# Optimization experiments

Hardware: AMD Instinct MI355X
Metric: run time of the kernel (lower is better)

## Reference

```python
import jax, jax.numpy as jnp
import numpy as np

VOCAB, B, T, H, E = 32000, 32, 128, 128, 128

def setup_inputs() -> dict:
    key = jax.random.key(0)
    ks = jax.random.split(key, 10)
    s = 0.05
    return {
        "inputs": jax.random.randint(ks[0], (B, T), 0, VOCAB, dtype=jnp.int32),
        "emb": jax.random.normal(ks[1], (VOCAB, E), jnp.float32) * s,
        "W0": jax.random.normal(ks[2], (E, 4 * H), jnp.float32) * s,
        "U0": jax.random.normal(ks[3], (H, 4 * H), jnp.float32) * s,
        "b0": jnp.zeros((4 * H,), jnp.float32),
        "W1": jax.random.normal(ks[4], (H, 4 * H), jnp.float32) * s,
        "U1": jax.random.normal(ks[5], (H, 4 * H), jnp.float32) * s,
        "b1": jnp.zeros((4 * H,), jnp.float32),
        "Wd": jax.random.normal(ks[6], (H, VOCAB), jnp.float32) * s,
        "bd": jnp.zeros((VOCAB,), jnp.float32),
    }

def _lstm_cell(x, h, c, W, U, b):
    # Keras LSTMCell gate order: i, f, c(candidate), o
    z = x @ W + h @ U + b  # [B, 4H]
    zi, zf, zc, zo = jnp.split(z, 4, axis=-1)
    i = jax.nn.sigmoid(zi)
    f = jax.nn.sigmoid(zf)
    o = jax.nn.sigmoid(zo)
    c_new = f * c + i * jnp.tanh(zc)
    h_new = o * jnp.tanh(c_new)
    return h_new, c_new

def reference(inputs, emb, W0, U0, b0, W1, U1, b1, Wd, bd):
    x = emb[inputs]  # [B, T, E]
    xt = jnp.transpose(x, (1, 0, 2))  # [T, B, E]
    zeros = jnp.zeros((x.shape[0], H), x.dtype)
    init = (zeros, zeros, zeros, zeros)  # h0, c0, h1, c1

    def step(carry, x_t):
        h0, c0, h1, c1 = carry
        h0, c0 = _lstm_cell(x_t, h0, c0, W0, U0, b0)
        h1, c1 = _lstm_cell(h0, h1, c1, W1, U1, b1)
        return (h0, c0, h1, c1), h1

    _, ys = jax.lax.scan(step, init, xt)  # ys: [T, B, H]
    y = jnp.transpose(ys, (1, 0, 2))  # [B, T, H]
    logits = y @ Wd + bd  # [B, T, VOCAB]
    return logits
```

## Files before the change

kernel.cpp:

```cpp
#include <hip/hip_runtime.h>
#include <math.h>

#define BB 32
#define TT 128
#define EE 128
#define HD 128
#define G4 512
#define NV 32000

typedef _Float16 f16x2 __attribute__((ext_vector_type(2)));
typedef _Float16 f16x8 __attribute__((ext_vector_type(8)));
typedef float    f32x4 __attribute__((ext_vector_type(4)));

__global__ __launch_bounds__(256) void k_prep(
    const int* __restrict__ inputs, const float* __restrict__ emb,
    const float* __restrict__ W0, const float* __restrict__ b0,
    float* __restrict__ Z0x,
    const float* __restrict__ Wd, _Float16* __restrict__ Whi, _Float16* __restrict__ Wlo)
{
    if (blockIdx.x < 2000) {
        const int g = blockIdx.x * 256 + threadIdx.x;
        const int chunk = g >> 6;
        const int lane = g & 63;
        const int ntile = chunk >> 2;
        const int kstep = chunk & 3;
        const int n = ntile * 16 + (lane & 15);
        const int kb = kstep * 32 + (lane >> 4) * 8;
        _Float16 hi[8], lo[8];
        #pragma unroll
        for (int j = 0; j < 8; ++j) {
            float v = Wd[(size_t)(kb + j) * NV + n];
            hi[j] = (_Float16)v;
            lo[j] = (_Float16)(v - (float)hi[j]);
        }
        *(float4*)&Whi[(size_t)chunk * 512 + lane * 8] = *(const float4*)hi;
        *(float4*)&Wlo[(size_t)chunk * 512 + lane * 8] = *(const float4*)lo;
        return;
    }
    __shared__ float xs[8][EE];
    const int r0 = (blockIdx.x - 2000) * 8;
    const int tid = threadIdx.x;
    for (int i = tid; i < 8 * EE; i += 256) {
        int r = i >> 7, e = i & 127;
        int tok = inputs[r0 + r];
        xs[r][e] = emb[tok * EE + e];
    }
    __syncthreads();
    const int c2 = tid * 2;
    float2 bb2 = *(const float2*)&b0[c2];
    float acc[8][2];
    #pragma unroll
    for (int r = 0; r < 8; ++r) { acc[r][0] = bb2.x; acc[r][1] = bb2.y; }
    for (int e = 0; e < EE; ++e) {
        float2 w = *(const float2*)&W0[e * G4 + c2];
        #pragma unroll
        for (int r = 0; r < 8; ++r) {
            float x = xs[r][e];
            acc[r][0] = fmaf(x, w.x, acc[r][0]);
            acc[r][1] = fmaf(x, w.y, acc[r][1]);
        }
    }
    #pragma unroll
    for (int r = 0; r < 8; ++r) {
        float2 o2; o2.x = acc[r][0]; o2.y = acc[r][1];
        *(float2*)&Z0x[(size_t)(r0 + r) * G4 + c2] = o2;
    }
}

__global__ __launch_bounds__(512, 2) void k_lstm_f(
    const float* __restrict__ Z0x,
    const float* __restrict__ U0, const float* __restrict__ W1,
    const float* __restrict__ U1, const float* __restrict__ b1,
    float* __restrict__ y)
{
    const int b = blockIdx.x;
    const int tid = threadIdx.x;

    __shared__ _Float16 h0p[HD];
    __shared__ _Float16 h1p[HD];
    __shared__ float zb[G4];
    __shared__ float zu[G4];

    f16x2 u0c[64], w1c[64], u1c[64];
    #pragma unroll
    for (int e2 = 0; e2 < 64; ++e2) {
        u0c[e2] = f16x2{(_Float16)U0[(2 * e2) * G4 + tid], (_Float16)U0[(2 * e2 + 1) * G4 + tid]};
        w1c[e2] = f16x2{(_Float16)W1[(2 * e2) * G4 + tid], (_Float16)W1[(2 * e2 + 1) * G4 + tid]};
        u1c[e2] = f16x2{(_Float16)U1[(2 * e2) * G4 + tid], (_Float16)U1[(2 * e2 + 1) * G4 + tid]};
    }

    const float b1c = b1[tid];
    const float* __restrict__ zrow = Z0x + (size_t)b * TT * G4 + tid;

    float c0 = 0.f, c1 = 0.f;
    if (tid < HD) { h0p[tid] = (_Float16)0.f; h1p[tid] = (_Float16)0.f; }
    __syncthreads();

    const f16x2* h0v = (const f16x2*)h0p;
    const f16x2* h1v = (const f16x2*)h1p;

    for (int t = 0; t < TT; ++t) {
        float a0a = zrow[(size_t)t * G4], a0b = 0.f;
        float aua = 0.f, aub = 0.f;
        #pragma unroll
        for (int e2 = 0; e2 < 64; e2 += 2) {
            a0a = __builtin_amdgcn_fdot2(h0v[e2],     u0c[e2],     a0a, false);
            a0b = __builtin_amdgcn_fdot2(h0v[e2 + 1], u0c[e2 + 1], a0b, false);
            aua = __builtin_amdgcn_fdot2(h1v[e2],     u1c[e2],     aua, false);
            aub = __builtin_amdgcn_fdot2(h1v[e2 + 1], u1c[e2 + 1], aub, false);
        }
        zb[tid] = a0a + a0b;
        zu[tid] = aua + aub;
        __syncthreads();

        if (tid < HD) {
            float zi = zb[tid], zf = zb[HD + tid], zc = zb[2 * HD + tid], zo = zb[3 * HD + tid];
            float ig = 1.f / (1.f + expf(-zi));
            float fg = 1.f / (1.f + expf(-zf));
            float og = 1.f / (1.f + expf(-zo));
            c0 = fg * c0 + ig * tanhf(zc);
            h0p[tid] = (_Float16)(og * tanhf(c0));
        }
        __syncthreads();

        float a1a = b1c + zu[tid], a1b = 0.f;
        #pragma unroll
        for (int e2 = 0; e2 < 64; e2 += 2) {
            a1a = __builtin_amdgcn_fdot2(h0v[e2],     w1c[e2],     a1a, false);
            a1b = __builtin_amdgcn_fdot2(h0v[e2 + 1], w1c[e2 + 1], a1b, false);
        }
        zb[tid] = a1a + a1b;
        __syncthreads();

        if (tid < HD) {
            float zi = zb[tid], zf = zb[HD + tid], zc = zb[2 * HD + tid], zo = zb[3 * HD + tid];
            float ig = 1.f / (1.f + expf(-zi));
            float fg = 1.f / (1.f + expf(-zf));
            float og = 1.f / (1.f + expf(-zo));
            c1 = fg * c1 + ig * tanhf(zc);
            float hn = og * tanhf(c1);
            h1p[tid] = (_Float16)hn;
            y[(size_t)(b * TT + t) * HD + tid] = hn;
        }
        __syncthreads();
    }
}

__global__ __launch_bounds__(256) void k_ysplit(
    const float* __restrict__ y, _Float16* __restrict__ yhi, _Float16* __restrict__ ylo)
{
    const int g = blockIdx.x * 256 + threadIdx.x;
    const int chunk = g >> 6;
    const int lane = g & 63;
    const int mtile = chunk >> 2;
    const int kstep = chunk & 3;
    const int row = mtile * 16 + (lane & 15);
    const int kb = kstep * 32 + (lane >> 4) * 8;
    _Float16 hi[8], lo[8];
    #pragma unroll
    for (int j = 0; j < 8; ++j) {
        float v = y[(size_t)row * HD + kb + j];
        hi[j] = (_Float16)v;
        lo[j] = (_Float16)(v - (float)hi[j]);
    }
    *(float4*)&yhi[(size_t)chunk * 512 + lane * 8] = *(const float4*)hi;
    *(float4*)&ylo[(size_t)chunk * 512 + lane * 8] = *(const float4*)lo;
}

__global__ __launch_bounds__(256) void k_dense_mfma(
    const _Float16* __restrict__ yhi, const _Float16* __restrict__ ylo,
    const _Float16* __restrict__ Whi, const _Float16* __restrict__ Wlo,
    const float* __restrict__ bd, float* __restrict__ out)
{
    const int tid = threadIdx.x;
    const int w = tid >> 6;
    const int lane = tid & 63;
    const int mtile = blockIdx.x * 4 + w;
    const int nt0 = blockIdx.y * 20;

    f16x8 Ah[4], Al[4];
    #pragma unroll
    for (int k = 0; k < 4; ++k) {
        Ah[k] = *(const f16x8*)&yhi[(size_t)(mtile * 4 + k) * 512 + lane * 8];
        Al[k] = *(const f16x8*)&ylo[(size_t)(mtile * 4 + k) * 512 + lane * 8];
    }

    const int m0 = mtile * 16;
    const int r0 = (lane >> 4) * 4;

    for (int nt = 0; nt < 20; ++nt) {
        const int ntile = nt0 + nt;
        const size_t cb = (size_t)ntile * 4 * 512 + lane * 8;
        f16x8 Bh[4], Bl[4];
        #pragma unroll
        for (int k = 0; k < 4; ++k) {
            Bh[k] = *(const f16x8*)&Whi[cb + k * 512];
            Bl[k] = *(const f16x8*)&Wlo[cb + k * 512];
        }
        f32x4 acc0 = {0.f, 0.f, 0.f, 0.f};
        f32x4 acc1 = {0.f, 0.f, 0.f, 0.f};
        #pragma unroll
        for (int k = 0; k < 4; ++k) {
            acc0 = __builtin_amdgcn_mfma_f32_16x16x32_f16(Ah[k], Bh[k], acc0, 0, 0, 0);
            acc1 = __builtin_amdgcn_mfma_f32_16x16x32_f16(Ah[k], Bl[k], acc1, 0, 0, 0);
            acc1 = __builtin_amdgcn_mfma_f32_16x16x32_f16(Al[k], Bh[k], acc1, 0, 0, 0);
        }
        const int col = ntile * 16 + (lane & 15);
        const float bias = bd[col];
        #pragma unroll
        for (int reg = 0; reg < 4; ++reg) {
            out[(size_t)(m0 + r0 + reg) * NV + col] = acc0[reg] + acc1[reg] + bias;
        }
    }
}

__global__ __launch_bounds__(256) void k_dense(
    const float* __restrict__ y, const float* __restrict__ Wd,
    const float* __restrict__ bd, float* __restrict__ out)
{
    __shared__ float ys[64 * HD];
    const int r0 = blockIdx.x * 64;
    const int v0 = blockIdx.y * 128;
    const int tid = threadIdx.x;
    for (int idx = tid; idx < 64 * HD; idx += 256) ys[idx] = y[(size_t)r0 * HD + idx];
    __syncthreads();
    const int tx = tid & 31;
    const int ty = tid >> 5;
    const int v = v0 + tx * 4;
    float4 bd4 = *(const float4*)&bd[v];
    float acc[8][4] = {};
    const float* yrow = &ys[(ty * 8) * HD];
    #pragma unroll 4
    for (int e = 0; e < HD; ++e) {
        float4 wv = *(const float4*)&Wd[(size_t)e * NV + v];
        #pragma unroll
        for (int j = 0; j < 8; ++j) {
            float yv = yrow[j * HD + e];
            acc[j][0] = fmaf(yv, wv.x, acc[j][0]);
            acc[j][1] = fmaf(yv, wv.y, acc[j][1]);
            acc[j][2] = fmaf(yv, wv.z, acc[j][2]);
            acc[j][3] = fmaf(yv, wv.w, acc[j][3]);
        }
    }
    #pragma unroll
    for (int j = 0; j < 8; ++j) {
        int rr = r0 + ty * 8 + j;
        float4 o4;
        o4.x = acc[j][0] + bd4.x;
        o4.y = acc[j][1] + bd4.y;
        o4.z = acc[j][2] + bd4.z;
        o4.w = acc[j][3] + bd4.w;
        *(float4*)&out[(size_t)rr * NV + v] = o4;
    }
}

extern "C" void kernel_launch(void* const* d_in, const int* in_sizes, int n_in,
                              void* d_out, int out_size, void* d_ws, size_t ws_size,
                              hipStream_t stream)
{
    const int*   inputs = (const int*)  d_in[0];
    const float* emb    = (const float*)d_in[1];
    const float* W0     = (const float*)d_in[2];
    const float* U0     = (const float*)d_in[3];
    const float* b0     = (const float*)d_in[4];
    const float* W1     = (const float*)d_in[5];
    const float* U1     = (const float*)d_in[6];
    const float* b1     = (const float*)d_in[7];
    const float* Wd     = (const float*)d_in[8];
    const float* bd     = (const float*)d_in[9];
    float* out = (float*)d_out;

    const size_t Z0X_B = (size_t)8 * 1024 * 1024;
    const size_t YY_B  = (size_t)2 * 1024 * 1024;
    const size_t WSP_B = (size_t)8000 * 512 * 2;
    const size_t YSP_B = (size_t)1024 * 512 * 2;
    const size_t NEED  = Z0X_B + YY_B + 2 * WSP_B + 2 * YSP_B + 4096;

    char* ws = (char*)d_ws;

    if (ws_size >= NEED) {
        float*     Z0x = (float*)ws;
        float*     yy  = (float*)(ws + Z0X_B);
        _Float16*  Whi = (_Float16*)(ws + Z0X_B + YY_B);
        _Float16*  Wlo = (_Float16*)(ws + Z0X_B + YY_B + WSP_B);
        _Float16*  yhi = (_Float16*)(ws + Z0X_B + YY_B + 2 * WSP_B);
        _Float16*  ylo = (_Float16*)(ws + Z0X_B + YY_B + 2 * WSP_B + YSP_B);

        k_prep<<<2512, 256, 0, stream>>>(inputs, emb, W0, b0, Z0x, Wd, Whi, Wlo);
        k_lstm_f<<<BB, 512, 0, stream>>>(Z0x, U0, W1, U1, b1, yy);
        k_ysplit<<<256, 256, 0, stream>>>(yy, yhi, ylo);
        k_dense_mfma<<<dim3(64, 100), 256, 0, stream>>>(yhi, ylo, Whi, Wlo, bd, out);
    } else {
        float* yy = (float*)ws;
        size_t out_bytes = (size_t)out_size * sizeof(float);
        float* Z0x = (float*)((char*)d_out + out_bytes - Z0X_B);

        k_prep<<<2512, 256, 0, stream>>>(inputs, emb, W0, b0, Z0x,
                                         Wd, (_Float16*)ws, (_Float16*)ws);
        k_lstm_f<<<BB, 512, 0, stream>>>(Z0x, U0, W1, U1, b1, yy);
        k_dense<<<dim3(64, 250), 256, 0, stream>>>(yy, Wd, bd, out);
    }
}
```

Before: 659.2 us.

## Halve LSTM block threads, two gate columns per thread with f16x8 vectorized dot loads

The recurrent LSTM kernel now runs 256 threads per block instead of 512. Each thread owns two gate columns and keeps 384 fp16 weights in registers. Hidden state is read from shared memory as f16x8 vectors, which cuts LDS load count and gives more independent dot-product chains per thread. The cost is much higher register pressure, with a risk of spills, and half as many waves to hide latency. Separately, the fallback path now skips the Wd split in k_prep by passing null pointers.

After: 917.5 us. +39.2%, slower.

```diff
diff --git a/kernel.cpp b/kernel.cpp
--- a/kernel.cpp
+++ b/kernel.cpp
@@ -19,6 +19,7 @@
     const float* __restrict__ Wd, _Float16* __restrict__ Whi, _Float16* __restrict__ Wlo)
 {
     if (blockIdx.x < 2000) {
+        if (Whi == nullptr) return;
         const int g = blockIdx.x * 256 + threadIdx.x;
         const int chunk = g >> 6;
         const int lane = g & 63;
@@ -67,7 +68,38 @@
     }
 }
 
-__global__ __launch_bounds__(512, 2) void k_lstm_f(
+#define REPEAT16(X) X(0) X(1) X(2) X(3) X(4) X(5) X(6) X(7) \
+                    X(8) X(9) X(10) X(11) X(12) X(13) X(14) X(15)
+
+#define D2(ACC, H, V, J) \
+    ACC = __builtin_amdgcn_fdot2(__builtin_shufflevector(H, H, 2*(J), 2*(J)+1), \
+                                 __builtin_shufflevector(V, V, 2*(J), 2*(J)+1), ACC, false)
+#define DOT8(ACC, H, V) do { D2(ACC,H,V,0); D2(ACC,H,V,1); D2(ACC,H,V,2); D2(ACC,H,V,3); } while (0)
+
+#define LDW(VAR, MAT, COL, I) do { \
+    f16x8 _v; \
+    _v[0] = (_Float16)MAT[((I)*8 + 0) * G4 + (COL)]; \
+    _v[1] = (_Float16)MAT[((I)*8 + 1) * G4 + (COL)]; \
+    _v[2] = (_Float16)MAT[((I)*8 + 2) * G4 + (COL)]; \
+    _v[3] = (_Float16)MAT[((I)*8 + 3) * G4 + (COL)]; \
+    _v[4] = (_Float16)MAT[((I)*8 + 4) * G4 + (COL)]; \
+    _v[5] = (_Float16)MAT[((I)*8 + 5) * G4 + (COL)]; \
+    _v[6] = (_Float16)MAT[((I)*8 + 6) * G4 + (COL)]; \
+    _v[7] = (_Float16)MAT[((I)*8 + 7) * G4 + (COL)]; \
+    VAR = _v; } while (0)
+
+#define DECLW(i) f16x8 u0a##i, u0b##i, u1a##i, u1b##i, w1a##i, w1b##i;
+#define LOADW(i) \
+    LDW(u0a##i, U0, ca, i); LDW(u0b##i, U0, cb, i); \
+    LDW(u1a##i, U1, ca, i); LDW(u1b##i, U1, cb, i); \
+    LDW(w1a##i, W1, ca, i); LDW(w1b##i, W1, cb, i);
+#define PHASEA(i) { f16x8 h0c = h0q[i]; DOT8(z0a, h0c, u0a##i); DOT8(z0b, h0c, u0b##i); \
+                    f16x8 h1c = h1q[i]; DOT8(zua, h1c, u1a##i); DOT8(zub, h1c, u1b##i); }
+#define PHASEC(i) { f16x8 h0c = h0q[i]; \
+                    DOT8((((i)&1) ? z1a2 : z1a1), h0c, w1a##i); \
+                    DOT8((((i)&1) ? z1b2 : z1b1), h0c, w1b##i); }
+
+__global__ __launch_bounds__(256, 1) void k_lstm_r2(
     const float* __restrict__ Z0x,
     const float* __restrict__ U0, const float* __restrict__ W1,
     const float* __restrict__ U1, const float* __restrict__ b1,
@@ -75,42 +107,34 @@
 {
     const int b = blockIdx.x;
     const int tid = threadIdx.x;
+    const int ca = tid;
+    const int cb = tid + 256;
 
     __shared__ _Float16 h0p[HD];
     __shared__ _Float16 h1p[HD];
     __shared__ float zb[G4];
     __shared__ float zu[G4];
 
-    f16x2 u0c[64], w1c[64], u1c[64];
-    #pragma unroll
-    for (int e2 = 0; e2 < 64; ++e2) {
-        u0c[e2] = f16x2{(_Float16)U0[(2 * e2) * G4 + tid], (_Float16)U0[(2 * e2 + 1) * G4 + tid]};
-        w1c[e2] = f16x2{(_Float16)W1[(2 * e2) * G4 + tid], (_Float16)W1[(2 * e2 + 1) * G4 + tid]};
-        u1c[e2] = f16x2{(_Float16)U1[(2 * e2) * G4 + tid], (_Float16)U1[(2 * e2 + 1) * G4 + tid]};
-    }
-
-    const float b1c = b1[tid];
-    const float* __restrict__ zrow = Z0x + (size_t)b * TT * G4 + tid;
+    REPEAT16(DECLW)
+    REPEAT16(LOADW)
+
+    const float b1a = b1[ca], b1b = b1[cb];
+    const float* __restrict__ zrow = Z0x + (size_t)b * TT * G4;
 
     float c0 = 0.f, c1 = 0.f;
     if (tid < HD) { h0p[tid] = (_Float16)0.f; h1p[tid] = (_Float16)0.f; }
     __syncthreads();
 
-    const f16x2* h0v = (const f16x2*)h0p;
-    const f16x2* h1v = (const f16x2*)h1p;
+    const f16x8* h0q = (const f16x8*)h0p;
+    const f16x8* h1q = (const f16x8*)h1p;
 
     for (int t = 0; t < TT; ++t) {
-        float a0a = zrow[(size_t)t * G4], a0b = 0.f;
-        float aua = 0.f, aub = 0.f;
-        #pragma unroll
-        for (int e2 = 0; e2 < 64; e2 += 2) {
-            a0a = __builtin_amdgcn_fdot2(h0v[e2],     u0c[e2],     a0a, false);
-            a0b = __builtin_amdgcn_fdot2(h0v[e2 + 1], u0c[e2 + 1], a0b, false);
-            aua = __builtin_amdgcn_fdot2(h1v[e2],     u1c[e2],     aua, false);
-            aub = __builtin_amdgcn_fdot2(h1v[e2 + 1], u1c[e2 + 1], aub, false);
-        }
-        zb[tid] = a0a + a0b;
-        zu[tid] = aua + aub;
+        float z0a = zrow[(size_t)t * G4 + ca];
+        float z0b = zrow[(size_t)t * G4 + cb];
+        float zua = 0.f, zub = 0.f;
+        REPEAT16(PHASEA)
+        zb[ca] = z0a; zb[cb] = z0b;
+        zu[ca] = zua; zu[cb] = zub;
         __syncthreads();
 
         if (tid < HD) {
@@ -123,13 +147,11 @@
         }
         __syncthreads();
 
-        float a1a = b1c + zu[tid], a1b = 0.f;
-        #pragma unroll
-        for (int e2 = 0; e2 < 64; e2 += 2) {
-            a1a = __builtin_amdgcn_fdot2(h0v[e2],     w1c[e2],     a1a, false);
-            a1b = __builtin_amdgcn_fdot2(h0v[e2 + 1], w1c[e2 + 1], a1b, false);
-        }
-        zb[tid] = a1a + a1b;
+        float z1a1 = b1a + zu[ca], z1a2 = 0.f;
+        float z1b1 = b1b + zu[cb], z1b2 = 0.f;
+        REPEAT16(PHASEC)
+        zb[ca] = z1a1 + z1a2;
+        zb[cb] = z1b1 + z1b2;
         __syncthreads();
 
         if (tid < HD) {
@@ -190,12 +212,12 @@
 
     for (int nt = 0; nt < 20; ++nt) {
         const int ntile = nt0 + nt;
-        const size_t cb = (size_t)ntile * 4 * 512 + lane * 8;
+        const size_t cbb = (size_t)ntile * 4 * 512 + lane * 8;
         f16x8 Bh[4], Bl[4];
         #pragma unroll
         for (int k = 0; k < 4; ++k) {
-            Bh[k] = *(const f16x8*)&Whi[cb + k * 512];
-            Bl[k] = *(const f16x8*)&Wlo[cb + k * 512];
+            Bh[k] = *(const f16x8*)&Whi[cbb + k * 512];
+            Bl[k] = *(const f16x8*)&Wlo[cbb + k * 512];
         }
         f32x4 acc0 = {0.f, 0.f, 0.f, 0.f};
         f32x4 acc1 = {0.f, 0.f, 0.f, 0.f};
@@ -287,7 +309,7 @@
         _Float16*  ylo = (_Float16*)(ws + Z0X_B + YY_B + 2 * WSP_B + YSP_B);
 
         k_prep<<<2512, 256, 0, stream>>>(inputs, emb, W0, b0, Z0x, Wd, Whi, Wlo);
-        k_lstm_f<<<BB, 512, 0, stream>>>(Z0x, U0, W1, U1, b1, yy);
+        k_lstm_r2<<<BB, 256, 0, stream>>>(Z0x, U0, W1, U1, b1, yy);
         k_ysplit<<<256, 256, 0, stream>>>(yy, yhi, ylo);
         k_dense_mfma<<<dim3(64, 100), 256, 0, stream>>>(yhi, ylo, Whi, Wlo, bd, out);
     } else {
@@ -296,8 +318,8 @@
         float* Z0x = (float*)((char*)d_out + out_bytes - Z0X_B);
 
         k_prep<<<2512, 256, 0, stream>>>(inputs, emb, W0, b0, Z0x,
-                                         Wd, (_Float16*)ws, (_Float16*)ws);
-        k_lstm_f<<<BB, 512, 0, stream>>>(Z0x, U0, W1, U1, b1, yy);
+                                         Wd, nullptr, nullptr);
+        k_lstm_r2<<<BB, 256, 0, stream>>>(Z0x, U0, W1, U1, b1, yy);
         k_dense<<<dim3(64, 250), 256, 0, stream>>>(yy, Wd, bd, out);
     }
 }
```

## Batch LSTM recurrence over 8 sequences per block with MFMA matmuls

Applied to the files above, without the earlier changes.

Replaces the per-sequence fdot2 LSTM kernel (32 blocks of 512 threads) with a kernel that processes 8 batch rows per block (4 blocks of 256 threads). The recurrent weights are kept as f16 MFMA fragments in registers, partly pinned to AGPRs, and the gate matmuls run as 16x16x32 MFMAs, with half of each 16-row tile left as padding. It also switches the activations to fast exp2/rcp approximations and fuses the layer-1 U1 matmul into the W1 pass. The sequential recurrence now runs on only 4 CUs, and per-step latency depends on MFMA chains and barriers. The fallback path now passes a null pointer so the prep kernel skips the split-weight work there.

New measurement: 606.8 us. 8.0% less time.

```diff
diff --git a/kernel.cpp b/kernel.cpp
--- a/kernel.cpp
+++ b/kernel.cpp
@@ -8,9 +8,10 @@
 #define G4 512
 #define NV 32000
 
-typedef _Float16 f16x2 __attribute__((ext_vector_type(2)));
-typedef _Float16 f16x8 __attribute__((ext_vector_type(8)));
-typedef float    f32x4 __attribute__((ext_vector_type(4)));
+typedef _Float16 f16x2  __attribute__((ext_vector_type(2)));
+typedef _Float16 f16x4v __attribute__((ext_vector_type(4)));
+typedef _Float16 f16x8  __attribute__((ext_vector_type(8)));
+typedef float    f32x4  __attribute__((ext_vector_type(4)));
 
 __global__ __launch_bounds__(256) void k_prep(
     const int* __restrict__ inputs, const float* __restrict__ emb,
@@ -19,6 +20,7 @@
     const float* __restrict__ Wd, _Float16* __restrict__ Whi, _Float16* __restrict__ Wlo)
 {
     if (blockIdx.x < 2000) {
+        if (Whi == nullptr) return;
         const int g = blockIdx.x * 256 + threadIdx.x;
         const int chunk = g >> 6;
         const int lane = g & 63;
@@ -67,80 +69,155 @@
     }
 }
 
-__global__ __launch_bounds__(512, 2) void k_lstm_f(
+__device__ __forceinline__ float sigf(float x) {
+    return __builtin_amdgcn_rcpf(1.f + __builtin_amdgcn_exp2f(x * -1.44269504088896f));
+}
+__device__ __forceinline__ float tanh_f(float x) {
+    return 1.f - 2.f * __builtin_amdgcn_rcpf(1.f + __builtin_amdgcn_exp2f(x * 2.88539008177793f));
+}
+__device__ __forceinline__ f16x8 ldfrag(const float* __restrict__ M, int col, int k0) {
+    f16x8 v;
+    #pragma unroll
+    for (int j = 0; j < 8; ++j) v[j] = (_Float16)M[(size_t)(k0 + j) * G4 + col];
+    return v;
+}
+
+#define REP8(X) X(0) X(1) X(2) X(3) X(4) X(5) X(6) X(7)
+
+#define MFMA(acc, a, b) acc = __builtin_amdgcn_mfma_f32_16x16x32_f16(a, b, acc, 0, 0, 0)
+
+#define DECLF(n) f16x8 u0_##n##_0, u0_##n##_1, u0_##n##_2, u0_##n##_3, \
+                       w1_##n##_0, w1_##n##_1, w1_##n##_2, w1_##n##_3, \
+                       u1_##n##_0, u1_##n##_1, u1_##n##_2, u1_##n##_3;
+
+#define LOADF(n) { const int cn = wc0 + (n) * 16 + lo16; \
+    u0_##n##_0 = ldfrag(U0, cn, khi);      u0_##n##_1 = ldfrag(U0, cn, 32 + khi); \
+    u0_##n##_2 = ldfrag(U0, cn, 64 + khi); u0_##n##_3 = ldfrag(U0, cn, 96 + khi); \
+    w1_##n##_0 = ldfrag(W1, cn, khi);      w1_##n##_1 = ldfrag(W1, cn, 32 + khi); \
+    w1_##n##_2 = ldfrag(W1, cn, 64 + khi); w1_##n##_3 = ldfrag(W1, cn, 96 + khi); \
+    asm("" : "+a"(w1_##n##_0), "+a"(w1_##n##_1), "+a"(w1_##n##_2), "+a"(w1_##n##_3)); \
+    u1_##n##_0 = ldfrag(U1, cn, khi);      u1_##n##_1 = ldfrag(U1, cn, 32 + khi); \
+    u1_##n##_2 = ldfrag(U1, cn, 64 + khi); u1_##n##_3 = ldfrag(U1, cn, 96 + khi); \
+    asm("" : "+a"(u1_##n##_0), "+a"(u1_##n##_1), "+a"(u1_##n##_2), "+a"(u1_##n##_3)); }
+
+#define PA(n) { f32x4 acc = {0.f, 0.f, 0.f, 0.f}; \
+    MFMA(acc, ha0, u0_##n##_0); MFMA(acc, ha1, u0_##n##_1); \
+    MFMA(acc, ha2, u0_##n##_2); MFMA(acc, ha3, u0_##n##_3); \
+    if (lane < 32) { const int cw = wc0 + (n) * 16 + lo16; const int br = (lane >> 4) * 4; \
+        zbuf[br + 0][cw] = acc[0]; zbuf[br + 1][cw] = acc[1]; \
+        zbuf[br + 2][cw] = acc[2]; zbuf[br + 3][cw] = acc[3]; } }
+
+#define PC(n) { f32x4 acc = {0.f, 0.f, 0.f, 0.f}; \
+    MFMA(acc, ha0, w1_##n##_0); MFMA(acc, ha1, w1_##n##_1); \
+    MFMA(acc, ha2, w1_##n##_2); MFMA(acc, ha3, w1_##n##_3); \
+    MFMA(acc, hb0, u1_##n##_0); MFMA(acc, hb1, u1_##n##_1); \
+    MFMA(acc, hb2, u1_##n##_2); MFMA(acc, hb3, u1_##n##_3); \
+    if (lane < 32) { const int cw = wc0 + (n) * 16 + lo16; const int br = (lane >> 4) * 4; \
+        zbuf[br + 0][cw] = acc[0]; zbuf[br + 1][cw] = acc[1]; \
+        zbuf[br + 2][cw] = acc[2]; zbuf[br + 3][cw] = acc[3]; } }
+
+#define GT0(K, ZI, ZF, ZC, ZO) { \
+    float ig = sigf(ZI), fg = sigf(ZF), og = sigf(ZO), gg = tanh_f(ZC); \
+    float cn = fg * c0v[K] + ig * gg; c0v[K] = cn; hv[K] = (_Float16)(og * tanh_f(cn)); }
+
+#define GT1(K, ZI, ZF, ZC, ZO, YO) { \
+    float ig = sigf(ZI), fg = sigf(ZF), og = sigf(ZO), gg = tanh_f(ZC); \
+    float cn = fg * c1v[K] + ig * gg; c1v[K] = cn; float hn = og * tanh_f(cn); \
+    hv[K] = (_Float16)hn; YO = hn; }
+
+__global__ __launch_bounds__(256, 1) void k_lstm_m(
     const float* __restrict__ Z0x,
     const float* __restrict__ U0, const float* __restrict__ W1,
     const float* __restrict__ U1, const float* __restrict__ b1,
     float* __restrict__ y)
 {
-    const int b = blockIdx.x;
-    const int tid = threadIdx.x;
-
-    __shared__ _Float16 h0p[HD];
-    __shared__ _Float16 h1p[HD];
-    __shared__ float zb[G4];
-    __shared__ float zu[G4];
-
-    f16x2 u0c[64], w1c[64], u1c[64];
-    #pragma unroll
-    for (int e2 = 0; e2 < 64; ++e2) {
-        u0c[e2] = f16x2{(_Float16)U0[(2 * e2) * G4 + tid], (_Float16)U0[(2 * e2 + 1) * G4 + tid]};
-        w1c[e2] = f16x2{(_Float16)W1[(2 * e2) * G4 + tid], (_Float16)W1[(2 * e2 + 1) * G4 + tid]};
-        u1c[e2] = f16x2{(_Float16)U1[(2 * e2) * G4 + tid], (_Float16)U1[(2 * e2 + 1) * G4 + tid]};
-    }
-
-    const float b1c = b1[tid];
-    const float* __restrict__ zrow = Z0x + (size_t)b * TT * G4 + tid;
-
-    float c0 = 0.f, c1 = 0.f;
-    if (tid < HD) { h0p[tid] = (_Float16)0.f; h1p[tid] = (_Float16)0.f; }
+    const int tid  = threadIdx.x;
+    const int lane = tid & 63;
+    const int wc0  = (tid >> 6) * 128;
+    const int lo16 = lane & 15;
+    const int khi  = (lane >> 4) * 8;
+    const int B0   = blockIdx.x * 8;
+
+    __shared__ float     zbuf[8][516];
+    __shared__ _Float16  h0p[16][136];
+    __shared__ _Float16  h1p[16][136];
+
+    REP8(DECLF)
+    REP8(LOADF)
+
+    const int bq  = tid >> 5;
+    const int h0i = (tid & 31) * 4;
+    const float* zx_base = Z0x + ((size_t)(B0 + bq) * TT) * G4;
+    float*       y_base  = y   + ((size_t)(B0 + bq) * TT) * HD + h0i;
+
+    const float4 b1_i = *(const float4*)&b1[0 * 128 + h0i];
+    const float4 b1_f = *(const float4*)&b1[1 * 128 + h0i];
+    const float4 b1_c = *(const float4*)&b1[2 * 128 + h0i];
+    const float4 b1_o = *(const float4*)&b1[3 * 128 + h0i];
+
+    for (int i = tid; i < 16 * 136; i += 256) {
+        ((_Float16*)h0p)[i] = (_Float16)0.f;
+        ((_Float16*)h1p)[i] = (_Float16)0.f;
+    }
+    f32x4 c0v = {0.f, 0.f, 0.f, 0.f};
+    f32x4 c1v = {0.f, 0.f, 0.f, 0.f};
     __syncthreads();
 
-    const f16x2* h0v = (const f16x2*)h0p;
-    const f16x2* h1v = (const f16x2*)h1p;
-
     for (int t = 0; t < TT; ++t) {
-        float a0a = zrow[(size_t)t * G4], a0b = 0.f;
-        float aua = 0.f, aub = 0.f;
-        #pragma unroll
-        for (int e2 = 0; e2 < 64; e2 += 2) {
-            a0a = __builtin_amdgcn_fdot2(h0v[e2],     u0c[e2],     a0a, false);
-            a0b = __builtin_amdgcn_fdot2(h0v[e2 + 1], u0c[e2 + 1], a0b, false);
-            aua = __builtin_amdgcn_fdot2(h1v[e2],     u1c[e2],     aua, false);
-            aub = __builtin_amdgcn_fdot2(h1v[e2 + 1], u1c[e2 + 1], aub, false);
-        }
-        zb[tid] = a0a + a0b;
-        zu[tid] = aua + aub;
+        const float* zx = zx_base + (size_t)t * G4;
+        const float4 x_i = *(const float4*)&zx[0 * 128 + h0i];
+        const float4 x_f = *(const float4*)&zx[1 * 128 + h0i];
+        const float4 x_c = *(const float4*)&zx[2 * 128 + h0i];
+        const float4 x_o = *(const float4*)&zx[3 * 128 + h0i];
+
+        {
+            f16x8 ha0 = *(const f16x8*)&h0p[lo16][khi];
+            f16x8 ha1 = *(const f16x8*)&h0p[lo16][32 + khi];
+            f16x8 ha2 = *(const f16x8*)&h0p[lo16][64 + khi];
+            f16x8 ha3 = *(const f16x8*)&h0p[lo16][96 + khi];
+            REP8(PA)
+        }
         __syncthreads();
 
-        if (tid < HD) {
-            float zi = zb[tid], zf = zb[HD + tid], zc = zb[2 * HD + tid], zo = zb[3 * HD + tid];
-            float ig = 1.f / (1.f + expf(-zi));
-            float fg = 1.f / (1.f + expf(-zf));
-            float og = 1.f / (1.f + expf(-zo));
-            c0 = fg * c0 + ig * tanhf(zc);
-            h0p[tid] = (_Float16)(og * tanhf(c0));
+        {
+            const float4 zi4 = *(const float4*)&zbuf[bq][0 * 128 + h0i];
+            const float4 zf4 = *(const float4*)&zbuf[bq][1 * 128 + h0i];
+            const float4 zc4 = *(const float4*)&zbuf[bq][2 * 128 + h0i];
+            const float4 zo4 = *(const float4*)&zbuf[bq][3 * 128 + h0i];
+            f16x4v hv;
+            GT0(0, zi4.x + x_i.x, zf4.x + x_f.x, zc4.x + x_c.x, zo4.x + x_o.x)
+            GT0(1, zi4.y + x_i.y, zf4.y + x_f.y, zc4.y + x_c.y, zo4.y + x_o.y)
+            GT0(2, zi4.z + x_i.z, zf4.z + x_f.z, zc4.z + x_c.z, zo4.z + x_o.z)
+            GT0(3, zi4.w + x_i.w, zf4.w + x_f.w, zc4.w + x_c.w, zo4.w + x_o.w)
+            *(f16x4v*)&h0p[bq][h0i] = hv;
         }
         __syncthreads();
 
-        float a1a = b1c + zu[tid], a1b = 0.f;
-        #pragma unroll
-        for (int e2 = 0; e2 < 64; e2 += 2) {
-            a1a = __builtin_amdgcn_fdot2(h0v[e2],     w1c[e2],     a1a, false);
-            a1b = __builtin_amdgcn_fdot2(h0v[e2 + 1], w1c[e2 + 1], a1b, false);
-        }
-        zb[tid] = a1a + a1b;
+        {
+            f16x8 ha0 = *(const f16x8*)&h0p[lo16][khi];
+            f16x8 ha1 = *(const f16x8*)&h0p[lo16][32 + khi];
+            f16x8 ha2 = *(const f16x8*)&h0p[lo16][64 + khi];
+            f16x8 ha3 = *(const f16x8*)&h0p[lo16][96 + khi];
+            f16x8 hb0 = *(const f16x8*)&h1p[lo16][khi];
+            f16x8 hb1 = *(const f16x8*)&h1p[lo16][32 + khi];
+            f16x8 hb2 = *(const f16x8*)&h1p[lo16][64 + khi];
+            f16x8 hb3 = *(const f16x8*)&h1p[lo16][96 + khi];
+            REP8(PC)
+        }
         __syncthreads();
 
-        if (tid < HD) {
-            float zi = zb[tid], zf = zb[HD + tid], zc = zb[2 * HD + tid], zo = zb[3 * HD + tid];
-            float ig = 1.f / (1.f + expf(-zi));
-            float fg = 1.f / (1.f + expf(-zf));
-            float og = 1.f / (1.f + expf(-zo));
-            c1 = fg * c1 + ig * tanhf(zc);
-            float hn = og * tanhf(c1);
-            h1p[tid] = (_Float16)hn;
-            y[(size_t)(b * TT + t) * HD + tid] = hn;
+        {
+            const float4 zi4 = *(const float4*)&zbuf[bq][0 * 128 + h0i];
+            const float4 zf4 = *(const float4*)&zbuf[bq][1 * 128 + h0i];
+            const float4 zc4 = *(const float4*)&zbuf[bq][2 * 128 + h0i];
+            const float4 zo4 = *(const float4*)&zbuf[bq][3 * 128 + h0i];
+            f16x4v hv; float4 yv;
+            GT1(0, zi4.x + b1_i.x, zf4.x + b1_f.x, zc4.x + b1_c.x, zo4.x + b1_o.x, yv.x)
+            GT1(1, zi4.y + b1_i.y, zf4.y + b1_f.y, zc4.y + b1_c.y, zo4.y + b1_o.y, yv.y)
+            GT1(2, zi4.z + b1_i.z, zf4.z + b1_f.z, zc4.z + b1_c.z, zo4.z + b1_o.z, yv.z)
+            GT1(3, zi4.w + b1_i.w, zf4.w + b1_f.w, zc4.w + b1_c.w, zo4.w + b1_o.w, yv.w)
+            *(f16x4v*)&h1p[bq][h0i] = hv;
+            *(float4*)(y_base + (size_t)t * HD) = yv;
         }
         __syncthreads();
     }
@@ -190,12 +267,12 @@
 
     for (int nt = 0; nt < 20; ++nt) {
         const int ntile = nt0 + nt;
-        const size_t cb = (size_t)ntile * 4 * 512 + lane * 8;
+        const size_t cbb = (size_t)ntile * 4 * 512 + lane * 8;
         f16x8 Bh[4], Bl[4];
         #pragma unroll
         for (int k = 0; k < 4; ++k) {
-            Bh[k] = *(const f16x8*)&Whi[cb + k * 512];
-            Bl[k] = *(const f16x8*)&Wlo[cb + k * 512];
+            Bh[k] = *(const f16x8*)&Whi[cbb + k * 512];
+            Bl[k] = *(const f16x8*)&Wlo[cbb + k * 512];
         }
         f32x4 acc0 = {0.f, 0.f, 0.f, 0.f};
         f32x4 acc1 = {0.f, 0.f, 0.f, 0.f};
@@ -287,7 +364,7 @@
         _Float16*  ylo = (_Float16*)(ws + Z0X_B + YY_B + 2 * WSP_B + YSP_B);
 
         k_prep<<<2512, 256, 0, stream>>>(inputs, emb, W0, b0, Z0x, Wd, Whi, Wlo);
-        k_lstm_f<<<BB, 512, 0, stream>>>(Z0x, U0, W1, U1, b1, yy);
+        k_lstm_m<<<4, 256, 0, stream>>>(Z0x, U0, W1, U1, b1, yy);
         k_ysplit<<<256, 256, 0, stream>>>(yy, yhi, ylo);
         k_dense_mfma<<<dim3(64, 100), 256, 0, stream>>>(yhi, ylo, Whi, Wlo, bd, out);
     } else {
@@ -296,8 +373,8 @@
         float* Z0x = (float*)((char*)d_out + out_bytes - Z0X_B);
 
         k_prep<<<2512, 256, 0, stream>>>(inputs, emb, W0, b0, Z0x,
-                                         Wd, (_Float16*)ws, (_Float16*)ws);
-        k_lstm_f<<<BB, 512, 0, stream>>>(Z0x, U0, W1, U1, b1, yy);
+                                         Wd, nullptr, nullptr);
+        k_lstm_m<<<4, 256, 0, stream>>>(Z0x, U0, W1, U1, b1, yy);
         k_dense<<<dim3(64, 250), 256, 0, stream>>>(yy, Wd, bd, out);
     }
 }
```
